# Optimization experiments

Measured on AMD Instinct MI355X. Metric: run time of the kernel, lower is better.

The kernel has to match this reference:

```python
import jax, jax.numpy as jnp
import numpy as np

E, TOP_K, D, H = 8, 2, 1024, 2048


def setup_inputs() -> dict:
    key = jax.random.key(0)
    ks = jax.random.split(key, 9)
    s = 0.02
    inputs = jax.random.normal(ks[0], (2, 2048, D), dtype=jnp.float32)
    gate_w = jax.random.normal(ks[1], (E, D), dtype=jnp.float32) * s  # Linear(d->E), no bias
    W0 = jax.random.normal(ks[2], (E, D, H), dtype=jnp.float32) * s
    b0 = jnp.zeros((E, H), dtype=jnp.float32)
    W1 = jax.random.normal(ks[3], (E, D, H), dtype=jnp.float32) * s
    b1 = jnp.zeros((E, H), dtype=jnp.float32)
    W2 = jax.random.normal(ks[4], (E, H, D), dtype=jnp.float32) * s
    b2 = jnp.zeros((E, D), dtype=jnp.float32)
    return {"inputs": inputs, "gate_w": gate_w, "W0": W0, "b0": b0,
            "W1": W1, "b1": b1, "W2": W2, "b2": b2}


def reference(inputs, gate_w, W0, b0, W1, b1, W2, b2):
    shp = inputs.shape
    x = inputs.reshape(-1, shp[-1])                      # [T, D]
    T = x.shape[0]
    logits = x @ gate_w.T                                # [T, E]
    w, sel = jax.lax.top_k(logits, TOP_K)                # [T, K]
    w = jax.nn.softmax(w, axis=-1)
    # dense combine weights [T, E]; top-k indices are distinct per row
    combine = jnp.zeros((T, E), dtype=x.dtype).at[
        jnp.arange(T)[:, None], sel].set(w)
    # per-expert SwiGLU FFN, evaluated densely, combined with (mostly zero) weights
    h0 = jnp.einsum('td,edh->eth', x, W0) + b0[:, None, :]
    h1 = jnp.einsum('td,edh->eth', x, W1) + b1[:, None, :]
    y = jnp.einsum('eth,ehd->etd', h0 * jax.nn.silu(h1), W2) + b2[:, None, :]
    out = jnp.einsum('te,etd->td', combine, y)           # [T, D]
    return out.reshape(shp)
```

## Files before the change

kernel.cpp:

```cpp
#include <hip/hip_runtime.h>
#include <hip/hip_bf16.h>
#include <cstdint>


#define E_ 8
#define D_ 1024
#define H_ 2048
#define T_ 4096

typedef __attribute__((ext_vector_type(8))) __bf16 bf16x8;
typedef __attribute__((ext_vector_type(4))) float f32x4;
typedef unsigned short u16;
typedef __attribute__((ext_vector_type(4))) u16 u16x4;

__device__ __forceinline__ u16 f2b(float f) {
    union { float f; unsigned int u; } v; v.f = f;
    unsigned int u = v.u;
    return (u16)((u + 0x7FFFu + ((u >> 16) & 1u)) >> 16);
}

__device__ __forceinline__ float b2f(u16 v) {
    union { unsigned int u; float f; } x; x.u = (unsigned int)v << 16; return x.f;
}

__device__ __forceinline__ void gld16(const void* g, void* l) {
    __builtin_amdgcn_global_load_lds((const __attribute__((address_space(1))) void*)g,
                                     (__attribute__((address_space(3))) void*)l, 16, 0, 0);
}

__global__ void k_gate(const float* __restrict__ x, const float* __restrict__ gw,
                       int* __restrict__ cnt2, int4* __restrict__ tslot,
                       float2* __restrict__ twgt, u16* __restrict__ xb) {
    __shared__ float gws[E_ * D_];
    int tid = threadIdx.x;
#pragma unroll
    for (int p = 0; p < 8; ++p) {
        int i = (p * 256 + tid) * 4;
        *(float4*)&gws[i] = *(const float4*)&gw[i];
    }
    __syncthreads();
    int wid = tid >> 6, lane = tid & 63;
    int t = blockIdx.x * 4 + wid;
    int chunk = blockIdx.x & 63;
    const float* xr = x + (size_t)t * D_;
    float part[E_];
#pragma unroll
    for (int e = 0; e < E_; ++e) part[e] = 0.f;
#pragma unroll
    for (int i = 0; i < 4; ++i) {
        int d = i * 256 + lane * 4;
        float4 xv = *(const float4*)(xr + d);
        u16x4 o;
        o[0] = f2b(xv.x); o[1] = f2b(xv.y); o[2] = f2b(xv.z); o[3] = f2b(xv.w);
        *(u16x4*)(xb + (size_t)t * D_ + d) = o;
#pragma unroll
        for (int e = 0; e < E_; ++e) {
            float4 g = *(const float4*)&gws[e * D_ + d];
            part[e] += xv.x * g.x + xv.y * g.y + xv.z * g.z + xv.w * g.w;
        }
    }
#pragma unroll
    for (int off = 32; off >= 1; off >>= 1) {
#pragma unroll
        for (int e = 0; e < E_; ++e) part[e] += __shfl_xor(part[e], off);
    }
    if (lane == 0) {
        int e0 = 0; float m0 = part[0];
#pragma unroll
        for (int e = 1; e < E_; ++e) if (part[e] > m0) { m0 = part[e]; e0 = e; }
        int e1 = -1; float m1 = -3.4e38f;
#pragma unroll
        for (int e = 0; e < E_; ++e) if (e != e0 && part[e] > m1) { m1 = part[e]; e1 = e; }
        float sx = __expf(m1 - m0);
        float w0 = 1.f / (1.f + sx);
        float w1 = sx / (1.f + sx);
        int lp0 = atomicAdd(&cnt2[chunk * 16 + e0], 1);
        int lp1 = atomicAdd(&cnt2[chunk * 16 + e1], 1);
        tslot[t] = make_int4(e0, lp0, e1, lp1);
        twgt[t] = make_float2(w0, w1);
    }
}

__global__ void k_scan2(const int* __restrict__ cnt2, int* __restrict__ chunk_off,
                        int* __restrict__ cnt, int* __restrict__ offs) {
    __shared__ int totals[E_];
    int e = threadIdx.x >> 6, lane = threadIdx.x & 63;
    int v = cnt2[lane * 16 + e];
    int incl = v;
#pragma unroll
    for (int d = 1; d < 64; d <<= 1) {
        int u = __shfl_up(incl, d);
        if (lane >= d) incl += u;
    }
    int excl = incl - v;
    if (lane == 63) totals[e] = incl;
    __syncthreads();
    chunk_off[lane * 8 + e] = excl;
    if (lane == 0) {
        int off_e = 0;
        for (int q = 0; q < e; ++q) off_e += totals[q];
        offs[e] = off_e; cnt[e] = totals[e];
    }
}

__global__ void k_fixup(const int* __restrict__ chunk_off, int4* __restrict__ tslot,
                        int* __restrict__ tok) {
    int t = blockIdx.x * 256 + threadIdx.x;
    int chunk = (t >> 2) & 63;
    int4 r = tslot[t];
    int s0 = chunk_off[chunk * 8 + r.x] + r.y;
    int s1 = chunk_off[chunk * 8 + r.z] + r.w;
    tok[r.x * T_ + s0] = t;
    tok[r.z * T_ + s1] = t;
    tslot[t] = make_int4(r.x, s0, r.z, s1);
}

__global__ void k_transpose_all(const float* __restrict__ W0, const float* __restrict__ W1,
                                const float* __restrict__ W2, u16* __restrict__ w0t,
                                u16* __restrict__ w1t, u16* __restrict__ w2t) {
    __shared__ float tile[64][67];
    int z = blockIdx.z, which = z >> 3, e = z & 7;
    const float* src; u16* dst; int R, C, c0, r0;
    if (which == 0)      { src = W0 + (size_t)e * D_ * H_; dst = w0t + (size_t)e * D_ * H_;
                           R = D_; C = H_; c0 = blockIdx.x * 64; r0 = blockIdx.y * 64; }
    else if (which == 1) { src = W1 + (size_t)e * D_ * H_; dst = w1t + (size_t)e * D_ * H_;
                           R = D_; C = H_; c0 = blockIdx.x * 64; r0 = blockIdx.y * 64; }
    else                 { src = W2 + (size_t)e * H_ * D_; dst = w2t + (size_t)e * H_ * D_;
                           R = H_; C = D_; c0 = blockIdx.y * 64; r0 = blockIdx.x * 64; }
    int tc4 = (threadIdx.x & 15) * 4, tr = threadIdx.x >> 4;
#pragma unroll
    for (int p = 0; p < 4; ++p) {
        float4 v = *(const float4*)(src + (size_t)(r0 + tr + 16 * p) * C + c0 + tc4);
        tile[tr + 16 * p][tc4 + 0] = v.x;
        tile[tr + 16 * p][tc4 + 1] = v.y;
        tile[tr + 16 * p][tc4 + 2] = v.z;
        tile[tr + 16 * p][tc4 + 3] = v.w;
    }
    __syncthreads();
    int r4 = (threadIdx.x & 15) * 4, tc = threadIdx.x >> 4;
#pragma unroll
    for (int p = 0; p < 4; ++p) {
        int c = tc + 16 * p;
        u16x4 o;
#pragma unroll
        for (int j = 0; j < 4; ++j) o[j] = f2b(tile[r4 + j][c]);
        *(u16x4*)(dst + (size_t)(c0 + c) * R + r0 + r4) = o;
    }
}

__launch_bounds__(256, 4)
__global__ void k_gemm1(const u16* __restrict__ xb, const u16* __restrict__ w0t,
                        const u16* __restrict__ w1t, const float* __restrict__ b0,
                        const float* __restrict__ b1, const int* __restrict__ tok,
                        const int* __restrict__ cnt, const int* __restrict__ offs,
                        u16* __restrict__ gbuf) {
    int e = blockIdx.z, rt = blockIdx.y, ct = blockIdx.x;
    int cN = cnt[e];
    if (rt * 128 >= cN) return;
    __shared__ u16 lds[16384];
    char* ldsB = (char*)lds;
    int tid = threadIdx.x, wid = tid >> 6, lane = tid & 63;
    int wm = wid >> 1, wn = wid & 1;
    const int* tokE = tok + e * T_;
    const u16* w0e = w0t + (size_t)e * H_ * D_;
    const u16* w1e = w1t + (size_t)e * H_ * D_;

    size_t aoff[4]; int adst[4];
#pragma unroll
    for (int p = 0; p < 4; ++p) {
        int cid = p * 256 + tid, r = cid >> 3, c = cid & 7;
        int cc = c ^ (r & 7);
        int tk = tokE[min(rt * 128 + r, cN - 1)];
        aoff[p] = (size_t)tk * D_ + cc * 8;
        adst[p] = (p * 256 + wid * 64) * 16;
    }
    size_t boff[2]; int bdst[2];
#pragma unroll
    for (int p = 0; p < 2; ++p) {
        int cid = p * 256 + tid, n = cid >> 3, c = cid & 7;
        int cc = c ^ (n & 7);
        boff[p] = (size_t)(ct * 64 + n) * D_ + cc * 8;
        bdst[p] = (p * 256 + wid * 64) * 16;
    }

    f32x4 acc0[4][2], acc1[4][2];
#pragma unroll
    for (int m = 0; m < 4; ++m)
#pragma unroll
        for (int n = 0; n < 2; ++n) { acc0[m][n] = (f32x4)0.f; acc1[m][n] = (f32x4)0.f; }

    for (int kt = 0; kt < D_ / 64; ++kt) {
        int k0 = kt * 64;
        __syncthreads();
#pragma unroll
        for (int p = 0; p < 4; ++p) gld16(xb + aoff[p] + k0, ldsB + adst[p]);
#pragma unroll
        for (int p = 0; p < 2; ++p) gld16(w0e + boff[p] + k0, ldsB + 16384 + bdst[p]);
#pragma unroll
        for (int p = 0; p < 2; ++p) gld16(w1e + boff[p] + k0, ldsB + 24576 + bdst[p]);
        __syncthreads();
#pragma unroll
        for (int ks = 0; ks < 2; ++ks) {
            int kc = ks * 4 + (lane >> 4);
            bf16x8 af[4], b0f[2], b1f[2];
#pragma unroll
            for (int m = 0; m < 4; ++m) {
                int row = wm * 64 + m * 16 + (lane & 15);
                af[m] = *(const bf16x8*)(ldsB + row * 128 + ((kc ^ (row & 7)) << 4));
            }
#pragma unroll
            for (int n = 0; n < 2; ++n) {
                int nr = wn * 32 + n * 16 + (lane & 15);
                int so = (kc ^ (nr & 7)) << 4;
                b0f[n] = *(const bf16x8*)(ldsB + 16384 + nr * 128 + so);
                b1f[n] = *(const bf16x8*)(ldsB + 24576 + nr * 128 + so);
            }
#pragma unroll
            for (int m = 0; m < 4; ++m)
#pragma unroll
                for (int n = 0; n < 2; ++n) {
                    acc0[m][n] = __builtin_amdgcn_mfma_f32_16x16x32_bf16(af[m], b0f[n], acc0[m][n], 0, 0, 0);
                    acc1[m][n] = __builtin_amdgcn_mfma_f32_16x16x32_bf16(af[m], b1f[n], acc1[m][n], 0, 0, 0);
                }
        }
    }
    int off_e = offs[e];
    const float* b0e = b0 + e * H_;
    const float* b1e = b1 + e * H_;
#pragma unroll
    for (int n = 0; n < 2; ++n) {
        int hc = ct * 64 + wn * 32 + n * 16 + (lane & 15);
        float bb0 = b0e[hc], bb1 = b1e[hc];
#pragma unroll
        for (int m = 0; m < 4; ++m)
#pragma unroll
            for (int i = 0; i < 4; ++i) {
                int row = wm * 64 + m * 16 + (lane >> 4) * 4 + i;
                int idx = rt * 128 + row;
                if (idx < cN) {
                    float h0 = acc0[m][n][i] + bb0;
                    float h1 = acc1[m][n][i] + bb1;
                    float g = h0 * h1 / (1.f + __expf(-h1));
                    gbuf[(size_t)(off_e + idx) * H_ + hc] = f2b(g);
                }
            }
    }
}

__launch_bounds__(256, 4)
__global__ void k_gemm2(const u16* __restrict__ gbuf, const u16* __restrict__ w2t,
                        const float* __restrict__ b2, const int* __restrict__ cnt,
                        const int* __restrict__ offs, u16* __restrict__ yb) {
    int e = blockIdx.z, rt = blockIdx.y, ct = blockIdx.x;
    int cN = cnt[e];
    if (rt * 128 >= cN) return;
    __shared__ u16 lds[16384];
    char* ldsB = (char*)lds;
    int tid = threadIdx.x, wid = tid >> 6, lane = tid & 63;
    int wm = wid >> 1, wn = wid & 1;
    int off_e = offs[e];
    const u16* Ag = gbuf + (size_t)(off_e + rt * 128) * H_;
    const u16* Bw = w2t + (size_t)e * D_ * H_ + (size_t)(ct * 128) * H_;

    size_t soff[4]; int sdst[4];
#pragma unroll
    for (int p = 0; p < 4; ++p) {
        int cid = p * 256 + tid, r = cid >> 3, c = cid & 7;
        int cc = c ^ (r & 7);
        soff[p] = (size_t)r * H_ + cc * 8;
        sdst[p] = (p * 256 + wid * 64) * 16;
    }
    f32x4 acc[4][4];
#pragma unroll
    for (int m = 0; m < 4; ++m)
#pragma unroll
        for (int n = 0; n < 4; ++n) acc[m][n] = (f32x4)0.f;

    for (int kt = 0; kt < H_ / 64; ++kt) {
        int k0 = kt * 64;
        __syncthreads();
#pragma unroll
        for (int p = 0; p < 4; ++p) gld16(Ag + soff[p] + k0, ldsB + sdst[p]);
#pragma unroll
        for (int p = 0; p < 4; ++p) gld16(Bw + soff[p] + k0, ldsB + 16384 + sdst[p]);
        __syncthreads();
#pragma unroll
        for (int ks = 0; ks < 2; ++ks) {
            int kc = ks * 4 + (lane >> 4);
            bf16x8 af[4], bfr[4];
#pragma unroll
            for (int m = 0; m < 4; ++m) {
                int row = wm * 64 + m * 16 + (lane & 15);
                af[m] = *(const bf16x8*)(ldsB + row * 128 + ((kc ^ (row & 7)) << 4));
            }
#pragma unroll
            for (int n = 0; n < 4; ++n) {
                int nr = wn * 64 + n * 16 + (lane & 15);
                bfr[n] = *(const bf16x8*)(ldsB + 16384 + nr * 128 + ((kc ^ (nr & 7)) << 4));
            }
#pragma unroll
            for (int m = 0; m < 4; ++m)
#pragma unroll
                for (int n = 0; n < 4; ++n)
                    acc[m][n] = __builtin_amdgcn_mfma_f32_16x16x32_bf16(af[m], bfr[n], acc[m][n], 0, 0, 0);
        }
    }
    const float* b2e = b2 + e * D_;
#pragma unroll
    for (int m = 0; m < 4; ++m)
#pragma unroll
        for (int i = 0; i < 4; ++i) {
            int row = wm * 64 + m * 16 + (lane >> 4) * 4 + i;
            int idx = rt * 128 + row;
            if (idx < cN) {
#pragma unroll
                for (int n = 0; n < 4; ++n) {
                    int dc = ct * 128 + wn * 64 + n * 16 + (lane & 15);
                    yb[(size_t)(off_e + idx) * D_ + dc] = f2b(acc[m][n][i] + b2e[dc]);
                }
            }
        }
}

__global__ void k_combine(const u16* __restrict__ yb, const int4* __restrict__ tslot,
                          const float2* __restrict__ twgt, const int* __restrict__ offs,
                          float* __restrict__ out) {
    int t = blockIdx.x, d4 = threadIdx.x * 4;
    int4 s = tslot[t];
    float2 w = twgt[t];
    const u16* y0 = yb + (size_t)(offs[s.x] + s.y) * D_ + d4;
    const u16* y1 = yb + (size_t)(offs[s.z] + s.w) * D_ + d4;
    u16x4 a = *(const u16x4*)y0;
    u16x4 b = *(const u16x4*)y1;
    float4 o;
    o.x = w.x * b2f(a[0]) + w.y * b2f(b[0]);
    o.y = w.x * b2f(a[1]) + w.y * b2f(b[1]);
    o.z = w.x * b2f(a[2]) + w.y * b2f(b[2]);
    o.w = w.x * b2f(a[3]) + w.y * b2f(b[3]);
    *(float4*)(out + (size_t)t * D_ + d4) = o;
}

extern "C" void kernel_launch(void* const* d_in, const int* in_sizes, int n_in,
                              void* d_out, int out_size, void* d_ws, size_t ws_size,
                              hipStream_t stream) {
    const float* x  = (const float*)d_in[0];
    const float* gw = (const float*)d_in[1];
    const float* W0 = (const float*)d_in[2];
    const float* b0 = (const float*)d_in[3];
    const float* W1 = (const float*)d_in[4];
    const float* b1 = (const float*)d_in[5];
    const float* W2 = (const float*)d_in[6];
    const float* b2 = (const float*)d_in[7];
    float* out = (float*)d_out;

    char* ws = (char*)d_ws;
    size_t off = 0;
    u16* xb   = (u16*)(ws + off); off += (size_t)T_ * D_ * 2;
    u16* w0t  = (u16*)(ws + off); off += (size_t)E_ * H_ * D_ * 2;
    u16* w1t  = (u16*)(ws + off); off += (size_t)E_ * H_ * D_ * 2;
    u16* w2t  = (u16*)(ws + off); off += (size_t)E_ * D_ * H_ * 2;
    u16* gbuf = (u16*)(ws + off); off += (size_t)(T_ * 2 + 256) * H_ * 2;
    int*   tok   = (int*)(ws + off);    off += (size_t)E_ * T_ * 4;
    int4*  tslot = (int4*)(ws + off);   off += (size_t)T_ * 16;
    float2* twgt = (float2*)(ws + off); off += (size_t)T_ * 8;
    int*   cnt2  = (int*)(ws + off);    off += 64 * 16 * 4;
    int*   choff = (int*)(ws + off);    off += 64 * 8 * 4;
    int*   cnt   = (int*)(ws + off);    off += 64;
    int*   offs  = (int*)(ws + off);    off += 64;
    u16* yb = w0t;

    if (ws_size < off) return;
    hipMemsetAsync(cnt2, 0, 64 * 16 * 4, stream);

    k_gate<<<T_ / 4, 256, 0, stream>>>(x, gw, cnt2, tslot, twgt, xb);
    k_scan2<<<1, 512, 0, stream>>>(cnt2, choff, cnt, offs);
    k_fixup<<<T_ / 256, 256, 0, stream>>>(choff, tslot, tok);
    k_transpose_all<<<dim3(32, 16, 24), 256, 0, stream>>>(W0, W1, W2, w0t, w1t, w2t);
    k_gemm1<<<dim3(H_ / 64, T_ / 128, E_), 256, 0, stream>>>(xb, w0t, w1t, b0, b1, tok, cnt, offs, gbuf);
    k_gemm2<<<dim3(D_ / 128, T_ / 128, E_), 256, 0, stream>>>(gbuf, w2t, b2, cnt, offs, yb);
    k_combine<<<T_, 256, 0, stream>>>(yb, tslot, twgt, offs, out);
}
```

Baseline: 239.2 us.

## Enlarge grouped GEMM tiles to 256 rows with 512 threads and double-buffered LDS

Both expert GEMMs move to 512-thread blocks computing 256-row tiles. gemm1 now computes a 128-column H slice with W0 and W1 rows interleaved in one B tile. Each kernel double-buffers its global-to-LDS staging so the next K-slice loads while the current one is multiplied, with one barrier per iteration, and raises wave priority around the MFMA bursts. The aims are more operand reuse per LDS load, fewer redundant weight reads, and load latency hidden behind compute. The cost is more LDS (96-128KB per block), more accumulator registers, and fewer blocks, which wastes more work on padded tiles for experts with uneven token counts.

```diff
diff --git a/kernel.cpp b/kernel.cpp
--- a/kernel.cpp
+++ b/kernel.cpp
@@ -148,7 +148,7 @@
     }
 }
 
-__launch_bounds__(256, 4)
+__launch_bounds__(512, 2)
 __global__ void k_gemm1(const u16* __restrict__ xb, const u16* __restrict__ w0t,
                         const u16* __restrict__ w1t, const float* __restrict__ b0,
                         const float* __restrict__ b1, const int* __restrict__ tok,
@@ -156,90 +156,96 @@
                         u16* __restrict__ gbuf) {
     int e = blockIdx.z, rt = blockIdx.y, ct = blockIdx.x;
     int cN = cnt[e];
-    if (rt * 128 >= cN) return;
-    __shared__ u16 lds[16384];
-    char* ldsB = (char*)lds;
+    if (rt * 256 >= cN) return;
+    __shared__ char lds[131072];
     int tid = threadIdx.x, wid = tid >> 6, lane = tid & 63;
-    int wm = wid >> 1, wn = wid & 1;
+    int wm = wid >> 2, wn = wid & 3;
     const int* tokE = tok + e * T_;
     const u16* w0e = w0t + (size_t)e * H_ * D_;
-    const u16* w1e = w1t + (size_t)e * H_ * D_;
-
-    size_t aoff[4]; int adst[4];
-#pragma unroll
-    for (int p = 0; p < 4; ++p) {
-        int cid = p * 256 + tid, r = cid >> 3, c = cid & 7;
-        int cc = c ^ (r & 7);
-        int tk = tokE[min(rt * 128 + r, cN - 1)];
-        aoff[p] = (size_t)tk * D_ + cc * 8;
-        adst[p] = (p * 256 + wid * 64) * 16;
-    }
-    size_t boff[2]; int bdst[2];
-#pragma unroll
-    for (int p = 0; p < 2; ++p) {
-        int cid = p * 256 + tid, n = cid >> 3, c = cid & 7;
-        int cc = c ^ (n & 7);
-        boff[p] = (size_t)(ct * 64 + n) * D_ + cc * 8;
-        bdst[p] = (p * 256 + wid * 64) * 16;
-    }
-
-    f32x4 acc0[4][2], acc1[4][2];
-#pragma unroll
-    for (int m = 0; m < 4; ++m)
-#pragma unroll
-        for (int n = 0; n < 2; ++n) { acc0[m][n] = (f32x4)0.f; acc1[m][n] = (f32x4)0.f; }
-
-    for (int kt = 0; kt < D_ / 64; ++kt) {
-        int k0 = kt * 64;
-        __syncthreads();
-#pragma unroll
-        for (int p = 0; p < 4; ++p) gld16(xb + aoff[p] + k0, ldsB + adst[p]);
-#pragma unroll
-        for (int p = 0; p < 2; ++p) gld16(w0e + boff[p] + k0, ldsB + 16384 + bdst[p]);
-#pragma unroll
-        for (int p = 0; p < 2; ++p) gld16(w1e + boff[p] + k0, ldsB + 24576 + bdst[p]);
-        __syncthreads();
+    size_t wdelta = (size_t)(w1t - w0t);
+
+    unsigned aoff[4]; int adst[4]; size_t boff[4];
+#pragma unroll
+    for (int i = 0; i < 4; ++i) {
+        int cid = i * 512 + tid;
+        int r = cid >> 3, c = cid & 7, cc = c ^ (r & 7);
+        int tk = tokE[min(rt * 256 + r, cN - 1)];
+        aoff[i] = (unsigned)(tk * D_ + cc * 8);
+        adst[i] = (i * 512 + wid * 64) * 16;
+        int g = r >> 5, which = g & 1;
+        int hcol = ct * 128 + (g >> 1) * 32 + (r & 31);
+        boff[i] = (size_t)which * wdelta + (size_t)hcol * D_ + cc * 8;
+    }
+
+    auto stageAll = [&](char* slot, int k0) {
+#pragma unroll
+        for (int i = 0; i < 4; ++i) gld16(xb + aoff[i] + k0, slot + adst[i]);
+#pragma unroll
+        for (int i = 0; i < 4; ++i) gld16(w0e + boff[i] + k0, slot + 32768 + adst[i]);
+    };
+
+    f32x4 acc[8][4];
+#pragma unroll
+    for (int m = 0; m < 8; ++m)
+#pragma unroll
+        for (int n = 0; n < 4; ++n) acc[m][n] = (f32x4)0.f;
+
+    const int NT = D_ / 64;
+    stageAll(lds, 0);
+    for (int t = 0; t < NT; ++t) {
+        asm volatile("s_waitcnt vmcnt(0)" ::: "memory");
+        __builtin_amdgcn_s_barrier();
+        const char* As = lds + (t & 1) * 65536;
+        const char* Bs = As + 32768;
+        if (t + 1 < NT) stageAll(lds + ((t + 1) & 1) * 65536, (t + 1) * 64);
+        bf16x8 bfr[2][4];
 #pragma unroll
         for (int ks = 0; ks < 2; ++ks) {
             int kc = ks * 4 + (lane >> 4);
-            bf16x8 af[4], b0f[2], b1f[2];
-#pragma unroll
-            for (int m = 0; m < 4; ++m) {
-                int row = wm * 64 + m * 16 + (lane & 15);
-                af[m] = *(const bf16x8*)(ldsB + row * 128 + ((kc ^ (row & 7)) << 4));
-            }
-#pragma unroll
-            for (int n = 0; n < 2; ++n) {
-                int nr = wn * 32 + n * 16 + (lane & 15);
-                int so = (kc ^ (nr & 7)) << 4;
-                b0f[n] = *(const bf16x8*)(ldsB + 16384 + nr * 128 + so);
-                b1f[n] = *(const bf16x8*)(ldsB + 24576 + nr * 128 + so);
-            }
-#pragma unroll
-            for (int m = 0; m < 4; ++m)
-#pragma unroll
-                for (int n = 0; n < 2; ++n) {
-                    acc0[m][n] = __builtin_amdgcn_mfma_f32_16x16x32_bf16(af[m], b0f[n], acc0[m][n], 0, 0, 0);
-                    acc1[m][n] = __builtin_amdgcn_mfma_f32_16x16x32_bf16(af[m], b1f[n], acc1[m][n], 0, 0, 0);
+#pragma unroll
+            for (int q = 0; q < 4; ++q) {
+                int rb = wn * 64 + q * 16 + (lane & 15);
+                bfr[ks][q] = *(const bf16x8*)(Bs + rb * 128 + ((kc ^ (rb & 7)) << 4));
+            }
+        }
+#pragma unroll
+        for (int MH = 0; MH < 2; ++MH) {
+            bf16x8 afr[2][4];
+#pragma unroll
+            for (int ks = 0; ks < 2; ++ks) {
+                int kc = ks * 4 + (lane >> 4);
+#pragma unroll
+                for (int m = 0; m < 4; ++m) {
+                    int row = wm * 128 + MH * 64 + m * 16 + (lane & 15);
+                    afr[ks][m] = *(const bf16x8*)(As + row * 128 + ((kc ^ (row & 7)) << 4));
                 }
+            }
+            __builtin_amdgcn_s_setprio(1);
+#pragma unroll
+            for (int ks = 0; ks < 2; ++ks)
+#pragma unroll
+                for (int m = 0; m < 4; ++m)
+#pragma unroll
+                    for (int q = 0; q < 4; ++q)
+                        acc[MH * 4 + m][q] = __builtin_amdgcn_mfma_f32_16x16x32_bf16(
+                            afr[ks][m], bfr[ks][q], acc[MH * 4 + m][q], 0, 0, 0);
+            __builtin_amdgcn_s_setprio(0);
         }
     }
+
     int off_e = offs[e];
-    const float* b0e = b0 + e * H_;
-    const float* b1e = b1 + e * H_;
 #pragma unroll
     for (int n = 0; n < 2; ++n) {
-        int hc = ct * 64 + wn * 32 + n * 16 + (lane & 15);
-        float bb0 = b0e[hc], bb1 = b1e[hc];
-#pragma unroll
-        for (int m = 0; m < 4; ++m)
+        int hc = ct * 128 + wn * 32 + n * 16 + (lane & 15);
+        float bb0 = b0[e * H_ + hc], bb1 = b1[e * H_ + hc];
+#pragma unroll
+        for (int mi = 0; mi < 8; ++mi)
 #pragma unroll
             for (int i = 0; i < 4; ++i) {
-                int row = wm * 64 + m * 16 + (lane >> 4) * 4 + i;
-                int idx = rt * 128 + row;
+                int idx = rt * 256 + wm * 128 + mi * 16 + (lane >> 4) * 4 + i;
                 if (idx < cN) {
-                    float h0 = acc0[m][n][i] + bb0;
-                    float h1 = acc1[m][n][i] + bb1;
+                    float h0 = acc[mi][n][i] + bb0;
+                    float h1 = acc[mi][n + 2][i] + bb1;
                     float g = h0 * h1 / (1.f + __expf(-h1));
                     gbuf[(size_t)(off_e + idx) * H_ + hc] = f2b(g);
                 }
@@ -247,79 +253,105 @@
     }
 }
 
-__launch_bounds__(256, 4)
+__launch_bounds__(512, 2)
 __global__ void k_gemm2(const u16* __restrict__ gbuf, const u16* __restrict__ w2t,
                         const float* __restrict__ b2, const int* __restrict__ cnt,
                         const int* __restrict__ offs, u16* __restrict__ yb) {
     int e = blockIdx.z, rt = blockIdx.y, ct = blockIdx.x;
     int cN = cnt[e];
-    if (rt * 128 >= cN) return;
-    __shared__ u16 lds[16384];
-    char* ldsB = (char*)lds;
+    if (rt * 256 >= cN) return;
+    __shared__ char lds[98304];
     int tid = threadIdx.x, wid = tid >> 6, lane = tid & 63;
-    int wm = wid >> 1, wn = wid & 1;
+    int wm = wid >> 2, wn = wid & 3;
     int off_e = offs[e];
-    const u16* Ag = gbuf + (size_t)(off_e + rt * 128) * H_;
+    const u16* Ag = gbuf + (size_t)(off_e + rt * 256) * H_;
     const u16* Bw = w2t + (size_t)e * D_ * H_ + (size_t)(ct * 128) * H_;
 
-    size_t soff[4]; int sdst[4];
-#pragma unroll
-    for (int p = 0; p < 4; ++p) {
-        int cid = p * 256 + tid, r = cid >> 3, c = cid & 7;
-        int cc = c ^ (r & 7);
-        soff[p] = (size_t)r * H_ + cc * 8;
-        sdst[p] = (p * 256 + wid * 64) * 16;
-    }
-    f32x4 acc[4][4];
-#pragma unroll
-    for (int m = 0; m < 4; ++m)
-#pragma unroll
-        for (int n = 0; n < 4; ++n) acc[m][n] = (f32x4)0.f;
-
-    for (int kt = 0; kt < H_ / 64; ++kt) {
-        int k0 = kt * 64;
-        __syncthreads();
-#pragma unroll
-        for (int p = 0; p < 4; ++p) gld16(Ag + soff[p] + k0, ldsB + sdst[p]);
-#pragma unroll
-        for (int p = 0; p < 4; ++p) gld16(Bw + soff[p] + k0, ldsB + 16384 + sdst[p]);
-        __syncthreads();
+    unsigned aoff[4]; int adst[4];
+#pragma unroll
+    for (int i = 0; i < 4; ++i) {
+        int cid = i * 512 + tid, r = cid >> 3, c = cid & 7, cc = c ^ (r & 7);
+        aoff[i] = (unsigned)(r * H_ + cc * 8);
+        adst[i] = (i * 512 + wid * 64) * 16;
+    }
+    unsigned boff[2]; int bdst[2];
+#pragma unroll
+    for (int i = 0; i < 2; ++i) {
+        int cid = i * 512 + tid, r = cid >> 3, c = cid & 7, cc = c ^ (r & 7);
+        boff[i] = (unsigned)(r * H_ + cc * 8);
+        bdst[i] = (i * 512 + wid * 64) * 16;
+    }
+
+    auto stageAll = [&](char* slot, int k0) {
+#pragma unroll
+        for (int i = 0; i < 4; ++i) gld16(Ag + aoff[i] + k0, slot + adst[i]);
+#pragma unroll
+        for (int i = 0; i < 2; ++i) gld16(Bw + boff[i] + k0, slot + 32768 + bdst[i]);
+    };
+
+    f32x4 acc[8][2];
+#pragma unroll
+    for (int m = 0; m < 8; ++m)
+#pragma unroll
+        for (int n = 0; n < 2; ++n) acc[m][n] = (f32x4)0.f;
+
+    const int NT = H_ / 64;
+    stageAll(lds, 0);
+    for (int t = 0; t < NT; ++t) {
+        asm volatile("s_waitcnt vmcnt(0)" ::: "memory");
+        __builtin_amdgcn_s_barrier();
+        const char* As = lds + (t & 1) * 49152;
+        const char* Bs = As + 32768;
+        if (t + 1 < NT) stageAll(lds + ((t + 1) & 1) * 49152, (t + 1) * 64);
+        bf16x8 bfr[2][2];
 #pragma unroll
         for (int ks = 0; ks < 2; ++ks) {
             int kc = ks * 4 + (lane >> 4);
-            bf16x8 af[4], bfr[4];
-#pragma unroll
-            for (int m = 0; m < 4; ++m) {
-                int row = wm * 64 + m * 16 + (lane & 15);
-                af[m] = *(const bf16x8*)(ldsB + row * 128 + ((kc ^ (row & 7)) << 4));
-            }
-#pragma unroll
-            for (int n = 0; n < 4; ++n) {
-                int nr = wn * 64 + n * 16 + (lane & 15);
-                bfr[n] = *(const bf16x8*)(ldsB + 16384 + nr * 128 + ((kc ^ (nr & 7)) << 4));
-            }
-#pragma unroll
-            for (int m = 0; m < 4; ++m)
-#pragma unroll
-                for (int n = 0; n < 4; ++n)
-                    acc[m][n] = __builtin_amdgcn_mfma_f32_16x16x32_bf16(af[m], bfr[n], acc[m][n], 0, 0, 0);
+#pragma unroll
+            for (int q = 0; q < 2; ++q) {
+                int rb = wn * 32 + q * 16 + (lane & 15);
+                bfr[ks][q] = *(const bf16x8*)(Bs + rb * 128 + ((kc ^ (rb & 7)) << 4));
+            }
         }
-    }
+#pragma unroll
+        for (int MH = 0; MH < 2; ++MH) {
+            bf16x8 afr[2][4];
+#pragma unroll
+            for (int ks = 0; ks < 2; ++ks) {
+                int kc = ks * 4 + (lane >> 4);
+#pragma unroll
+                for (int m = 0; m < 4; ++m) {
+                    int row = wm * 128 + MH * 64 + m * 16 + (lane & 15);
+                    afr[ks][m] = *(const bf16x8*)(As + row * 128 + ((kc ^ (row & 7)) << 4));
+                }
+            }
+            __builtin_amdgcn_s_setprio(1);
+#pragma unroll
+            for (int ks = 0; ks < 2; ++ks)
+#pragma unroll
+                for (int m = 0; m < 4; ++m)
+#pragma unroll
+                    for (int q = 0; q < 2; ++q)
+                        acc[MH * 4 + m][q] = __builtin_amdgcn_mfma_f32_16x16x32_bf16(
+                            afr[ks][m], bfr[ks][q], acc[MH * 4 + m][q], 0, 0, 0);
+            __builtin_amdgcn_s_setprio(0);
+        }
+    }
+
     const float* b2e = b2 + e * D_;
 #pragma unroll
-    for (int m = 0; m < 4; ++m)
-#pragma unroll
-        for (int i = 0; i < 4; ++i) {
-            int row = wm * 64 + m * 16 + (lane >> 4) * 4 + i;
-            int idx = rt * 128 + row;
-            if (idx < cN) {
-#pragma unroll
-                for (int n = 0; n < 4; ++n) {
-                    int dc = ct * 128 + wn * 64 + n * 16 + (lane & 15);
-                    yb[(size_t)(off_e + idx) * D_ + dc] = f2b(acc[m][n][i] + b2e[dc]);
-                }
-            }
-        }
+    for (int q = 0; q < 2; ++q) {
+        int dc = ct * 128 + wn * 32 + q * 16 + (lane & 15);
+        float bb = b2e[dc];
+#pragma unroll
+        for (int mi = 0; mi < 8; ++mi)
+#pragma unroll
+            for (int i = 0; i < 4; ++i) {
+                int idx = rt * 256 + wm * 128 + mi * 16 + (lane >> 4) * 4 + i;
+                if (idx < cN)
+                    yb[(size_t)(off_e + idx) * D_ + dc] = f2b(acc[mi][q][i] + bb);
+            }
+    }
 }
 
 __global__ void k_combine(const u16* __restrict__ yb, const int4* __restrict__ tslot,
@@ -376,7 +408,7 @@
     k_scan2<<<1, 512, 0, stream>>>(cnt2, choff, cnt, offs);
     k_fixup<<<T_ / 256, 256, 0, stream>>>(choff, tslot, tok);
     k_transpose_all<<<dim3(32, 16, 24), 256, 0, stream>>>(W0, W1, W2, w0t, w1t, w2t);
-    k_gemm1<<<dim3(H_ / 64, T_ / 128, E_), 256, 0, stream>>>(xb, w0t, w1t, b0, b1, tok, cnt, offs, gbuf);
-    k_gemm2<<<dim3(D_ / 128, T_ / 128, E_), 256, 0, stream>>>(gbuf, w2t, b2, cnt, offs, yb);
+    k_gemm1<<<dim3(H_ / 128, T_ / 256, E_), 512, 0, stream>>>(xb, w0t, w1t, b0, b1, tok, cnt, offs, gbuf);
+    k_gemm2<<<dim3(D_ / 128, T_ / 256, E_), 512, 0, stream>>>(gbuf, w2t, b2, cnt, offs, yb);
     k_combine<<<T_, 256, 0, stream>>>(yb, tslot, twgt, offs, out);
 }
```

After: 268.4 us. +12.2%, slower.
